# Optimization experiments

Hardware: AMD Instinct MI355X
Metric: run time of the kernel (lower is better)

The kernel has to match this reference:

```python
import jax, jax.numpy as jnp
import numpy as np
from jax import lax

B, D, H, W = 2, 96, 96, 96
K = 3          # static upper bound on connected components (setup builds exactly 3 blobs)
CC_ITERS = 48  # >= max component diameter under 26-connectivity label propagation
V = D * H * W
BIGI = jnp.int32(V)  # sentinel label for background


def _make_target():
    # 3 well-separated spherical lesions per volume -> exactly K connected components
    centers = [(20, 20, 20), (70, 30, 60), (40, 75, 75)]
    r2 = 9 ** 2
    zz, yy, xx = np.meshgrid(np.arange(D), np.arange(H), np.arange(W), indexing='ij')
    vol = np.zeros((D, H, W), np.float32)
    for cz, cy, cx in centers:
        vol[(zz - cz) ** 2 + (yy - cy) ** 2 + (xx - cx) ** 2 <= r2] = 1.0
    return jnp.asarray(np.stack([vol, np.roll(vol, 5, axis=2)])[:, None])  # [B,1,D,H,W]


def setup_inputs() -> dict:
    key = jax.random.key(0)
    pred = jax.random.normal(key, (B, 1, D, H, W), jnp.float32)
    return {"pred": pred, "target": _make_target()}


def _connected_components(mask):
    # 26-connectivity labeling (matches skimage/cucim default for 3D).
    # Label = min flat raster index in each component, so ascending-sorted labels
    # reproduce cucim's scan-order labels 1..N (needed for tie-breaking parity).
    lab = jnp.where(mask, jnp.arange(V, dtype=jnp.int32).reshape(mask.shape), BIGI)
    for _ in range(CC_ITERS):  # fixed unroll; components have diameter << CC_ITERS
        nb = lax.reduce_window(lab, BIGI, lax.min, (3, 3, 3), (1, 1, 1), 'SAME')
        lab = jnp.where(mask, nb, BIGI)
    return lab


def _edt1d(f):
    # exact 1D squared-distance lower envelope: d[i] = min_j f[j] + (i-j)^2
    n = f.shape[-1]
    i = jnp.arange(n, dtype=jnp.float32)
    sq = (i[:, None] - i[None, :]) ** 2  # [n_out, n_in]
    return jnp.min(f[..., None, :] + sq, axis=-1)


def _squared_edt(seed):
    # exact squared Euclidean distance-to-seed via 3 separable passes
    f = jnp.where(seed, jnp.float32(0), jnp.float32(1e12))
    for ax in range(3):
        f = jnp.moveaxis(_edt1d(jnp.moveaxis(f, ax, -1)), -1, ax)
    return f


def _forward(pred, target):
    p = jax.nn.sigmoid(pred)[:, 0]  # dim==5 -> sigmoid; squeeze channel -> [B,D,H,W]
    g = target[:, 0]

    def labels(gt):
        lab = _connected_components(gt > 0.5)
        ul = jnp.unique(lab, size=K + 1, fill_value=BIGI)[:K]  # ascending = scan order
        return lab, ul

    lab, ul = jax.vmap(labels)(g)                 # lab [B,D,H,W], ul [B,K]
    valid = (ul < BIGI).astype(p.dtype)           # [B,K]
    seeds = lab[:, None] == ul[:, :, None, None, None]  # [B,K,D,H,W] bool
    # serial map over (B*K) regions keeps the [D,H,W,n] EDT intermediate to one at a time
    dists = lax.map(_squared_edt, seeds.reshape(B * K, D, H, W)).reshape(B, K, D, H, W)
    # squared vs sqrt distance: same ordering AND same ties as torch's strict '<' update;
    rmap = jnp.argmin(dists, axis=1)              # Voronoi region map [B,D,H,W]

    oh = jax.nn.one_hot(rmap, K, dtype=p.dtype)   # [B,D,H,W,K]
    inter = jnp.einsum('bdhw,bdhwk->bk', p * g, oh)
    psum = jnp.einsum('bdhw,bdhwk->bk', p, oh)
    gsum = jnp.einsum('bdhw,bdhwk->bk', g, oh)
    dice = 2.0 * inter / (psum + gsum + 1e-8)
    cnt = jnp.sum(valid, axis=1)
    mean_dice = jnp.sum(dice * valid, axis=1) / jnp.maximum(cnt, 1.0)
    loss = jnp.where(cnt > 0, 1.0 - mean_dice, 1.0)  # num_features==0 -> loss 1.0
    return jnp.mean(loss)


def reference(pred, target):
    return _forward(pred, target)
```

## Files before the change

### kernel.cpp

```cpp
#include <hip/hip_runtime.h>
#include <math.h>

#define SLICE 9216
#define VOL 884736
#define NB 2
#define KK 3
#define BIGI VOL
#define BIGP 0x3FFFFFFC
#define BIGPF 1.0e9f
#define CC_SWEEPS 4
#define NYC 4
#define NZC 4
#define NPART (NB*96*NZC)
#define MAXROW 64
#define MAXNZ 64
#define YSTR (MAXNZ*96)

#define OFF_ACT   (NB*VOL*4)
#define OFF_DISTC (2*NB*VOL*4)
#define DISTC_BYTES (NB*96*MAXNZ*96*4)
#define OFF_SMALL (OFF_DISTC + DISTC_BYTES)
#define OFF_ZMASK (OFF_SMALL + 64)
#define OFF_ROOTS (OFF_SMALL + 128)
#define OFF_MASK  (OFF_SMALL + 1024)
#define MASK_ULL  (NB*KK*96*96*2)
#define OFF_PART  (OFF_MASK + MASK_ULL*8)

__global__ void k_init(const float4* __restrict__ tgt4, int* __restrict__ lab,
                       int* __restrict__ act, int* __restrict__ small,
                       unsigned long long* __restrict__ masks) {
  int q = blockIdx.x * 256 + threadIdx.x;
  if (q < MASK_ULL) masks[q] = 0;
  if (q >= NB * VOL / 4) return;
  float4 tv = tgt4[q];
  int base = q * 4;
  int bo = (base >= VOL) ? VOL : 0;
  int4 lv;
  lv.x = (tv.x > 0.5f) ? base - bo     : BIGI;
  lv.y = (tv.y > 0.5f) ? base - bo + 1 : BIGI;
  lv.z = (tv.z > 0.5f) ? base - bo + 2 : BIGI;
  lv.w = (tv.w > 0.5f) ? base - bo + 3 : BIGI;
  ((int4*)lab)[q] = lv;
  int cnt = (lv.x != BIGI) + (lv.y != BIGI) + (lv.z != BIGI) + (lv.w != BIGI);
  if (cnt) {
    int pos = atomicAdd(&small[0], cnt);
    if (lv.x != BIGI) act[pos++] = base;
    if (lv.y != BIGI) act[pos++] = base + 1;
    if (lv.z != BIGI) act[pos++] = base + 2;
    if (lv.w != BIGI) act[pos]   = base + 3;
  }
}

__global__ void k_prop(int* __restrict__ lab, const int* __restrict__ act,
                       int* __restrict__ small, int record,
                       int* __restrict__ roots) {
  int n = small[0];
  for (int i = blockIdx.x * blockDim.x + threadIdx.x; i < n;
       i += gridDim.x * blockDim.x) {
    int idx = act[i];
    int bo = (idx >= VOL) ? VOL : 0;
    int v = idx - bo;
    int z = v / SLICE;
    int rem = v - z * SLICE;
    int y = rem / 96;
    int x = rem - y * 96;
    int* L = lab + bo;
    int z0 = z > 0 ? z - 1 : 0, z1 = z < 95 ? z + 1 : 95;
    int y0 = y > 0 ? y - 1 : 0, y1 = y < 95 ? y + 1 : 95;
    int x0 = x > 0 ? x - 1 : 0, x1 = x < 95 ? x + 1 : 95;
    int m = BIGI;
    for (int zz = z0; zz <= z1; zz++)
      for (int yy = y0; yy <= y1; yy++) {
        const int* row = L + zz * SLICE + yy * 96;
        for (int xx = x0; xx <= x1; xx++) m = min(m, row[xx]);
      }
    int m2 = L[m];
    int m3 = L[m2];
    lab[idx] = m3;
    if (record && m3 == v) {
      int b = bo ? 1 : 0;
      int pos = atomicAdd(&small[1 + b], 1);
      if (pos < 64) roots[b * 64 + pos] = v;
    }
  }
}

__global__ void k_seeds(const int* __restrict__ lab, const int* __restrict__ act,
                        const int* __restrict__ small, const int* __restrict__ roots,
                        unsigned long long* __restrict__ masks,
                        unsigned long long* __restrict__ zmg) {
  __shared__ int s_roots[128];
  __shared__ int s_ul[NB][KK];
  __shared__ unsigned long long zm[NB * 2];
  int t = threadIdx.x;
  if (t < 128) {
    int b = t >> 6, j = t & 63;
    int nr = small[1 + b]; if (nr > 64) nr = 64;
    s_roots[t] = (j < nr) ? roots[t] : 0x7fffffff;
  }
  if (t < NB * KK) s_ul[t / KK][t % KK] = -2;
  if (t < NB * 2) zm[t] = 0;
  __syncthreads();
  if (t < 128) {
    int r = s_roots[t];
    if (r != 0x7fffffff) {
      int b = t >> 6;
      int rank = 0;
      #pragma unroll
      for (int j = 0; j < 64; j++)
        rank += (s_roots[(b << 6) + j] < r) ? 1 : 0;
      if (rank < KK) s_ul[b][rank] = r;
    }
  }
  __syncthreads();
  int n = small[0];
  for (int i = blockIdx.x * 256 + t; i < n; i += gridDim.x * 256) {
    int idx = act[i];
    int b = (idx >= VOL) ? 1 : 0;
    int v = idx - (b ? VOL : 0);
    int lv = lab[idx];
    int k = (lv == s_ul[b][0]) ? 0 : (lv == s_ul[b][1]) ? 1
          : (lv == s_ul[b][2]) ? 2 : -1;
    if (k >= 0) {
      int z = v / SLICE;
      int rem = v - z * SLICE;
      int y = rem / 96;
      int x = rem - y * 96;
      unsigned long long* M =
          masks + (((size_t)(b * KK + k) * 96 + z) * 96 + y) * 2;
      if (x < 64) atomicOr(&M[0], 1ull << x);
      else        atomicOr(&M[1], 1ull << (x - 64));
      if (z < 64) atomicOr(&zm[b * 2],     1ull << z);
      else        atomicOr(&zm[b * 2 + 1], 1ull << (z - 64));
    }
  }
  __syncthreads();
  if (t < NB * 2 && zm[t]) atomicOr(&zmg[t], zm[t]);
}

__device__ __forceinline__ int row_dist(unsigned long long lo,
                                        unsigned long long hi, int x) {
  int dr, dlft;
  {
    unsigned long long rl, rh;
    if (x == 0)      { rl = lo; rh = hi; }
    else if (x < 64) { rl = (lo >> x) | (hi << (64 - x)); rh = hi >> x; }
    else             { rl = hi >> (x - 64); rh = 0; }
    dr = rl ? (__ffsll(rl) - 1) : (rh ? (63 + __ffsll(rh)) : 1000);
  }
  {
    unsigned long long ll, lh;
    if (x >= 64) { ll = lo; lh = hi & ((2ull << (x - 64)) - 1); }
    else         { ll = lo & ((2ull << x) - 1); lh = 0; }
    dlft = lh ? (x - 127 + __clzll(lh))
              : (ll ? (x - 63 + __clzll(ll)) : 1000);
  }
  return min(dr, dlft);
}

__global__ __launch_bounds__(256) void k_edt_xy(const unsigned long long* __restrict__ masks,
                                                const unsigned long long* __restrict__ zmg,
                                                float* __restrict__ distC) {
  int blk = blockIdx.x;
  int b = blk / (MAXNZ * NYC);
  int rem = blk - b * MAXNZ * NYC;
  int jj = rem / NYC;
  int yc = rem - jj * NYC;
  unsigned long long zlo = zmg[b * 2], zhi = zmg[b * 2 + 1];
  int nlo = __popcll(zlo);
  int nz = nlo + __popcll(zhi);
  if (jj >= nz) return;
  int z;
  if (jj < nlo) {
    unsigned long long w = zlo;
    for (int i = 0; i < jj; i++) w &= w - 1;
    z = __ffsll(w) - 1;
  } else {
    unsigned long long w = zhi;
    int r2 = jj - nlo;
    for (int i = 0; i < r2; i++) w &= w - 1;
    z = 64 + __ffsll(w) - 1;
  }
  __shared__ unsigned long long sM[KK * 192];
  __shared__ float pl[MAXROW * 96];
  __shared__ unsigned char vrow[96];
  __shared__ int s_n;
  int t = threadIdx.x;
  if (t == 0) s_n = 0;
  for (int i = t; i < KK * 192; i += 256) {
    int k = i / 192, r = i - k * 192;
    sM[i] = masks[((size_t)(b * KK + k) * 96 + z) * 192 + r];
  }
  __syncthreads();
  if (t < 96) {
    unsigned long long any = sM[t * 2] | sM[t * 2 + 1] | sM[192 + t * 2] |
                             sM[193 + t * 2] | sM[384 + t * 2] | sM[385 + t * 2];
    if (any) {
      int pos = atomicAdd(&s_n, 1);
      if (pos < MAXROW) vrow[pos] = (unsigned char)t;
    }
  }
  __syncthreads();
  int n = s_n; if (n > MAXROW) n = MAXROW;
  for (int i = t; i < n * 96; i += 256) {
    int j2 = i / 96, x = i - j2 * 96;
    int y = vrow[j2];
    int best = BIGP;
    #pragma unroll
    for (int k = 0; k < KK; k++) {
      unsigned long long lo = sM[k * 192 + y * 2];
      unsigned long long hi = sM[k * 192 + y * 2 + 1];
      if (lo | hi) {
        int d = row_dist(lo, hi, x);
        best = min(best, ((d * d) << 2) | k);
      }
    }
    pl[j2 * 96 + x] = (best == BIGP) ? BIGPF : (float)best;
  }
  __syncthreads();
  for (int tt = t; tt < 288; tt += 256) {
    int x = tt % 96;
    int yg = tt / 96;
    int yy0 = yc * 24 + yg * 8;
    float acc[8];
    #pragma unroll
    for (int i2 = 0; i2 < 8; i2++) acc[i2] = BIGPF;
    for (int j2 = 0; j2 < n; j2++) {
      int j = vrow[j2];
      float f = pl[j2 * 96 + x];
      float d0 = (float)(yy0 - j);
      #pragma unroll
      for (int i2 = 0; i2 < 8; i2++) {
        float dy = d0 + (float)i2;
        acc[i2] = fminf(acc[i2], __builtin_fmaf(4.f * dy, dy, f));
      }
    }
    float* DA = distC + (size_t)b * 96 * YSTR + jj * 96 + x;
    #pragma unroll
    for (int i2 = 0; i2 < 8; i2++)
      DA[(yy0 + i2) * YSTR] = acc[i2];
  }
}

__global__ __launch_bounds__(256) void k_z_fuse(const float* __restrict__ distC,
                                                const unsigned long long* __restrict__ zmg,
                                                const float* __restrict__ pred,
                                                const float* __restrict__ tgt,
                                                float* __restrict__ part,
                                                int* __restrict__ small,
                                                float* __restrict__ out) {
  int blk = blockIdx.x;
  int b = blk / (96 * NZC);
  int rem = blk - b * 96 * NZC;
  int y = rem / NZC;
  int zc = rem - y * NZC;
  __shared__ float g[MAXNZ * 96];
  __shared__ unsigned char zl[96];
  __shared__ int s_last;
  __shared__ float wsum[4][9];
  int t = threadIdx.x;
  if (t == 0) s_last = 0;
  unsigned long long zlo = zmg[b * 2], zhi = zmg[b * 2 + 1];
  int nz = __popcll(zlo) + __popcll(zhi);
  if (nz > MAXNZ) nz = MAXNZ;
  if (t < 96) {
    int set = (t < 64) ? (int)((zlo >> t) & 1) : (int)((zhi >> (t - 64)) & 1);
    if (set) {
      int jj;
      if (t < 64) jj = __popcll(zlo & ((t ? (1ull << t) : 1ull) - 1ull));
      else        jj = __popcll(zlo) + __popcll(zhi & ((1ull << (t - 64)) - 1ull));
      if (jj < MAXNZ) zl[jj] = (unsigned char)t;
    }
  }
  {
    const float4* src4 = (const float4*)(distC + (size_t)(b * 96 + y) * YSTR);
    float4* g4 = (float4*)g;
    int n4 = nz * 24;
    for (int i = t; i < n4; i += 256) g4[i] = src4[i];
  }
  __syncthreads();
  const float* P = pred + (size_t)b * VOL + y * 96;
  const float* G = tgt + (size_t)b * VOL + y * 96;
  float a0 = 0.f, a1 = 0.f, a2 = 0.f, a3 = 0.f, a4 = 0.f,
        a5 = 0.f, a6 = 0.f, a7 = 0.f, a8 = 0.f;
  for (int tt = t; tt < 288; tt += 256) {
    int x = tt % 96;
    int zg = tt / 96;
    int zz0 = zc * 24 + zg * 8;
    float pv[8], gv[8];
    #pragma unroll
    for (int i2 = 0; i2 < 8; i2++) {
      int off = (zz0 + i2) * SLICE + x;
      pv[i2] = P[off];
      gv[i2] = G[off];
    }
    float acc[8];
    #pragma unroll
    for (int i2 = 0; i2 < 8; i2++) acc[i2] = BIGPF;
    for (int jj = 0; jj < nz; jj++) {
      float f = g[jj * 96 + x];
      float d0 = (float)(zz0 - (int)zl[jj]);
      #pragma unroll
      for (int i2 = 0; i2 < 8; i2++) {
        float dz = d0 + (float)i2;
        acc[i2] = fminf(acc[i2], __builtin_fmaf(4.f * dz, dz, f));
      }
    }
    #pragma unroll
    for (int i2 = 0; i2 < 8; i2++) {
      float p = __builtin_amdgcn_rcpf(1.f + __expf(-pv[i2]));
      float gg = gv[i2];
      int kk = ((int)acc[i2]) & 3;
      float pg = p * gg;
      a0 += (kk == 0) ? pg : 0.f;
      a1 += (kk == 1) ? pg : 0.f;
      a2 += (kk == 2) ? pg : 0.f;
      a3 += (kk == 0) ? p : 0.f;
      a4 += (kk == 1) ? p : 0.f;
      a5 += (kk == 2) ? p : 0.f;
      a6 += (kk == 0) ? gg : 0.f;
      a7 += (kk == 1) ? gg : 0.f;
      a8 += (kk == 2) ? gg : 0.f;
    }
  }
  float s[9] = {a0, a1, a2, a3, a4, a5, a6, a7, a8};
  #pragma unroll
  for (int off = 32; off > 0; off >>= 1)
    #pragma unroll
    for (int q = 0; q < 9; q++) s[q] += __shfl_down(s[q], off);
  int wave = t >> 6, lane = t & 63;
  if (lane == 0) {
    #pragma unroll
    for (int q = 0; q < 9; q++) wsum[wave][q] = s[q];
  }
  __syncthreads();
  if (t < 9)
    part[blk * 9 + t] = wsum[0][t] + wsum[1][t] + wsum[2][t] + wsum[3][t];
  __syncthreads();
  if (t == 0) {
    __threadfence();
    int c = atomicAdd(&small[3], 1);
    s_last = (c == NPART - 1) ? 1 : 0;
  }
  __syncthreads();
  if (!s_last) return;
  __threadfence();
  float a[18];
  #pragma unroll
  for (int q = 0; q < 18; q++) a[q] = 0.f;
  for (int r = t; r < NPART; r += 256) {
    int bb = r / (96 * NZC);
    #pragma unroll
    for (int q = 0; q < 9; q++) a[bb * 9 + q] += part[r * 9 + q];
  }
  #pragma unroll
  for (int off = 32; off > 0; off >>= 1)
    #pragma unroll
    for (int q = 0; q < 18; q++) a[q] += __shfl_down(a[q], off);
  __shared__ float fs[4][18];
  if (lane == 0) {
    #pragma unroll
    for (int q = 0; q < 18; q++) fs[wave][q] = a[q];
  }
  __syncthreads();
  if (t == 0) {
    float tot[18];
    #pragma unroll
    for (int q = 0; q < 18; q++)
      tot[q] = fs[0][q] + fs[1][q] + fs[2][q] + fs[3][q];
    float loss = 0.f;
    for (int bb = 0; bb < NB; bb++) {
      int cnt = small[1 + bb];
      if (cnt > KK) cnt = KK;
      float ds = 0.f;
      for (int k = 0; k < cnt; k++) {
        float inter = tot[bb * 9 + k];
        float ps = tot[bb * 9 + 3 + k];
        float gs = tot[bb * 9 + 6 + k];
        ds += 2.f * inter / (ps + gs + 1e-8f);
      }
      float mean = ds / fmaxf((float)cnt, 1.f);
      loss += (cnt > 0) ? (1.f - mean) : 1.f;
    }
    out[0] = loss * 0.5f;
  }
}

extern "C" void kernel_launch(void* const* d_in, const int* in_sizes, int n_in,
                              void* d_out, int out_size, void* d_ws, size_t ws_size,
                              hipStream_t stream) {
  const float* pred = (const float*)d_in[0];
  const float* tgt  = (const float*)d_in[1];
  float* out = (float*)d_out;

  char* ws = (char*)d_ws;
  int* lab   = (int*)(ws);
  int* act   = (int*)(ws + OFF_ACT);
  float* distC = (float*)(ws + OFF_DISTC);
  int* small = (int*)(ws + OFF_SMALL);
  unsigned long long* zmg = (unsigned long long*)(ws + OFF_ZMASK);
  int* roots = (int*)(ws + OFF_ROOTS);
  unsigned long long* masks = (unsigned long long*)(ws + OFF_MASK);
  float* part = (float*)(ws + OFF_PART);

  hipMemsetAsync(ws + OFF_SMALL, 0, 128, stream);
  k_init<<<(NB * VOL / 4 + 255) / 256, 256, 0, stream>>>(
      (const float4*)tgt, lab, act, small, masks);
  for (int it = 0; it < CC_SWEEPS; it++)
    k_prop<<<96, 256, 0, stream>>>(lab, act, small, it == CC_SWEEPS - 1 ? 1 : 0, roots);
  k_seeds<<<96, 256, 0, stream>>>(lab, act, small, roots, masks, zmg);
  k_edt_xy<<<NB * MAXNZ * NYC, 256, 0, stream>>>(masks, zmg, distC);
  k_z_fuse<<<NB * 96 * NZC, 256, 0, stream>>>(distC, zmg, pred, tgt, part, small, out);
}
```

Before: 149.5 us.

## Replace atomic active-voxel list with dense int4 scans in propagation and seeding

Result: slower. 187.6 us (+25.4%).

```diff
diff --git a/kernel.cpp b/kernel.cpp
--- a/kernel.cpp
+++ b/kernel.cpp
@@ -15,9 +15,9 @@
 #define MAXROW 64
 #define MAXNZ 64
 #define YSTR (MAXNZ*96)
-
-#define OFF_ACT   (NB*VOL*4)
-#define OFF_DISTC (2*NB*VOL*4)
+#define NQ (NB*VOL/4)
+
+#define OFF_DISTC (NB*VOL*4)
 #define DISTC_BYTES (NB*96*MAXNZ*96*4)
 #define OFF_SMALL (OFF_DISTC + DISTC_BYTES)
 #define OFF_ZMASK (OFF_SMALL + 64)
@@ -27,11 +27,13 @@
 #define OFF_PART  (OFF_MASK + MASK_ULL*8)
 
 __global__ void k_init(const float4* __restrict__ tgt4, int* __restrict__ lab,
-                       int* __restrict__ act, int* __restrict__ small,
+                       int* __restrict__ small, unsigned long long* __restrict__ zmg,
                        unsigned long long* __restrict__ masks) {
   int q = blockIdx.x * 256 + threadIdx.x;
   if (q < MASK_ULL) masks[q] = 0;
-  if (q >= NB * VOL / 4) return;
+  if (q < 8) small[q] = 0;
+  if (q < 4) zmg[q] = 0;
+  if (q >= NQ) return;
   float4 tv = tgt4[q];
   int base = q * 4;
   int bo = (base >= VOL) ? VOL : 0;
@@ -41,30 +43,26 @@
   lv.z = (tv.z > 0.5f) ? base - bo + 2 : BIGI;
   lv.w = (tv.w > 0.5f) ? base - bo + 3 : BIGI;
   ((int4*)lab)[q] = lv;
-  int cnt = (lv.x != BIGI) + (lv.y != BIGI) + (lv.z != BIGI) + (lv.w != BIGI);
-  if (cnt) {
-    int pos = atomicAdd(&small[0], cnt);
-    if (lv.x != BIGI) act[pos++] = base;
-    if (lv.y != BIGI) act[pos++] = base + 1;
-    if (lv.z != BIGI) act[pos++] = base + 2;
-    if (lv.w != BIGI) act[pos]   = base + 3;
-  }
-}
-
-__global__ void k_prop(int* __restrict__ lab, const int* __restrict__ act,
-                       int* __restrict__ small, int record,
-                       int* __restrict__ roots) {
-  int n = small[0];
-  for (int i = blockIdx.x * blockDim.x + threadIdx.x; i < n;
-       i += gridDim.x * blockDim.x) {
-    int idx = act[i];
-    int bo = (idx >= VOL) ? VOL : 0;
-    int v = idx - bo;
+}
+
+__global__ void k_prop(int* __restrict__ lab, int* __restrict__ small,
+                       int* __restrict__ roots, int record) {
+  int q = blockIdx.x * 256 + threadIdx.x;
+  if (q >= NQ) return;
+  int4 lq = ((const int4*)lab)[q];
+  if (lq.x == BIGI && lq.y == BIGI && lq.z == BIGI && lq.w == BIGI) return;
+  int base = q * 4;
+  int bo = (base >= VOL) ? VOL : 0;
+  int* L = lab + bo;
+  #pragma unroll
+  for (int u = 0; u < 4; u++) {
+    int lvu = (u == 0) ? lq.x : (u == 1) ? lq.y : (u == 2) ? lq.z : lq.w;
+    if (lvu == BIGI) continue;
+    int v = base - bo + u;
     int z = v / SLICE;
     int rem = v - z * SLICE;
     int y = rem / 96;
     int x = rem - y * 96;
-    int* L = lab + bo;
     int z0 = z > 0 ? z - 1 : 0, z1 = z < 95 ? z + 1 : 95;
     int y0 = y > 0 ? y - 1 : 0, y1 = y < 95 ? y + 1 : 95;
     int x0 = x > 0 ? x - 1 : 0, x1 = x < 95 ? x + 1 : 95;
@@ -76,7 +74,7 @@
       }
     int m2 = L[m];
     int m3 = L[m2];
-    lab[idx] = m3;
+    L[v] = m3;
     if (record && m3 == v) {
       int b = bo ? 1 : 0;
       int pos = atomicAdd(&small[1 + b], 1);
@@ -85,8 +83,8 @@
   }
 }
 
-__global__ void k_seeds(const int* __restrict__ lab, const int* __restrict__ act,
-                        const int* __restrict__ small, const int* __restrict__ roots,
+__global__ void k_seeds(const int* __restrict__ lab, const int* __restrict__ small,
+                        const int* __restrict__ roots,
                         unsigned long long* __restrict__ masks,
                         unsigned long long* __restrict__ zmg) {
   __shared__ int s_roots[128];
@@ -113,25 +111,30 @@
     }
   }
   __syncthreads();
-  int n = small[0];
-  for (int i = blockIdx.x * 256 + t; i < n; i += gridDim.x * 256) {
-    int idx = act[i];
-    int b = (idx >= VOL) ? 1 : 0;
-    int v = idx - (b ? VOL : 0);
-    int lv = lab[idx];
-    int k = (lv == s_ul[b][0]) ? 0 : (lv == s_ul[b][1]) ? 1
-          : (lv == s_ul[b][2]) ? 2 : -1;
-    if (k >= 0) {
-      int z = v / SLICE;
-      int rem = v - z * SLICE;
-      int y = rem / 96;
-      int x = rem - y * 96;
-      unsigned long long* M =
-          masks + (((size_t)(b * KK + k) * 96 + z) * 96 + y) * 2;
-      if (x < 64) atomicOr(&M[0], 1ull << x);
-      else        atomicOr(&M[1], 1ull << (x - 64));
-      if (z < 64) atomicOr(&zm[b * 2],     1ull << z);
-      else        atomicOr(&zm[b * 2 + 1], 1ull << (z - 64));
+  int q = blockIdx.x * 256 + t;
+  if (q < NQ) {
+    int4 lq = ((const int4*)lab)[q];
+    int base = q * 4;
+    int b = (base >= VOL) ? 1 : 0;
+    #pragma unroll
+    for (int u = 0; u < 4; u++) {
+      int lv = (u == 0) ? lq.x : (u == 1) ? lq.y : (u == 2) ? lq.z : lq.w;
+      if (lv >= BIGI) continue;
+      int k = (lv == s_ul[b][0]) ? 0 : (lv == s_ul[b][1]) ? 1
+            : (lv == s_ul[b][2]) ? 2 : -1;
+      if (k >= 0) {
+        int v = base - (b ? VOL : 0) + u;
+        int z = v / SLICE;
+        int rem = v - z * SLICE;
+        int y = rem / 96;
+        int x = rem - y * 96;
+        unsigned long long* M =
+            masks + (((size_t)(b * KK + k) * 96 + z) * 96 + y) * 2;
+        if (x < 64) atomicOr(&M[0], 1ull << x);
+        else        atomicOr(&M[1], 1ull << (x - 64));
+        if (z < 64) atomicOr(&zm[b * 2],     1ull << z);
+        else        atomicOr(&zm[b * 2 + 1], 1ull << (z - 64));
+      }
     }
   }
   __syncthreads();
@@ -395,7 +398,6 @@
 
   char* ws = (char*)d_ws;
   int* lab   = (int*)(ws);
-  int* act   = (int*)(ws + OFF_ACT);
   float* distC = (float*)(ws + OFF_DISTC);
   int* small = (int*)(ws + OFF_SMALL);
   unsigned long long* zmg = (unsigned long long*)(ws + OFF_ZMASK);
@@ -403,12 +405,11 @@
   unsigned long long* masks = (unsigned long long*)(ws + OFF_MASK);
   float* part = (float*)(ws + OFF_PART);
 
-  hipMemsetAsync(ws + OFF_SMALL, 0, 128, stream);
-  k_init<<<(NB * VOL / 4 + 255) / 256, 256, 0, stream>>>(
-      (const float4*)tgt, lab, act, small, masks);
+  int nblk = (NQ + 255) / 256;
+  k_init<<<nblk, 256, 0, stream>>>((const float4*)tgt, lab, small, zmg, masks);
   for (int it = 0; it < CC_SWEEPS; it++)
-    k_prop<<<96, 256, 0, stream>>>(lab, act, small, it == CC_SWEEPS - 1 ? 1 : 0, roots);
-  k_seeds<<<96, 256, 0, stream>>>(lab, act, small, roots, masks, zmg);
+    k_prop<<<nblk, 256, 0, stream>>>(lab, small, roots, it == CC_SWEEPS - 1 ? 1 : 0);
+  k_seeds<<<nblk, 256, 0, stream>>>(lab, small, roots, masks, zmg);
   k_edt_xy<<<NB * MAXNZ * NYC, 256, 0, stream>>>(masks, zmg, distC);
   k_z_fuse<<<NB * 96 * NZC, 256, 0, stream>>>(distC, zmg, pred, tgt, part, small, out);
 }
```
